# Performance work log

Hardware: AMD Instinct MI355X
Metric: run time of the kernel (lower is better)

Reference implementation:

```python
import jax, jax.numpy as jnp
import numpy as np

NOS = 4          # number of species (experts)
IN = 128         # descriptor size
H1 = 32
H2 = 32
N_ATOMS = 500000


def setup_inputs() -> dict:
    key = jax.random.key(0)
    ks = jax.random.split(key, 8)
    desc = jax.random.normal(ks[0], (N_ATOMS, IN), dtype=jnp.float32)
    species = jax.random.randint(ks[1], (N_ATOMS,), 0, NOS, dtype=jnp.int64)
    s = 0.05  # small init scale
    W0 = jax.random.normal(ks[2], (NOS, IN, H1), dtype=jnp.float32) * s
    b0 = jax.random.normal(ks[3], (NOS, H1), dtype=jnp.float32) * s
    W1 = jax.random.normal(ks[4], (NOS, H1, H2), dtype=jnp.float32) * s
    b1 = jax.random.normal(ks[5], (NOS, H2), dtype=jnp.float32) * s
    W2 = jax.random.normal(ks[6], (NOS, H2, 1), dtype=jnp.float32) * s
    b2 = jax.random.normal(ks[7], (NOS, 1), dtype=jnp.float32) * s
    return {"desc": desc, "species": species, "W0": W0, "b0": b0,
            "W1": W1, "b1": b1, "W2": W2, "b2": b2}


def reference(desc, species, W0, b0, W1, b1, W2, b2):
    # Run every species MLP on all atoms (NOS is small), then select per
    # atom's species and sum -> total energy. Same math as predict_E.
    # h: [s, n, h1]
    h = jnp.tanh(jnp.einsum('ni,sih->snh', desc, W0) + b0[:, None, :])
    h = jnp.tanh(jnp.einsum('snh,sho->sno', h, W1) + b1[:, None, :])
    out = jnp.einsum('snh,sho->sno', h, W2) + b2[:, None, :]   # [s, n, 1]
    per_atom = jnp.take_along_axis(out[..., 0], species[None, :], axis=0)[0]
    return jnp.sum(per_atom)
```

## Files before the change

### kernel.cpp

```cpp
#include <hip/hip_runtime.h>
#include <hip/hip_bf16.h>


#define NATOMS 500000
#define NSPEC  4
#define DIN    128
#define DH1    32
#define DH2    32

#define IDX_CAP 500064
#define T_MAX   (IDX_CAP / 16)

#define OFF_COUNTS 0
#define OFF_CURS   16
#define OFF_BASES  32
#define OFF_IDX    256
#define OFF_FRAG   2000640
#define SPEC_STRIDE 11840

typedef __bf16 bf16x8 __attribute__((ext_vector_type(8)));
typedef float  f32x4  __attribute__((ext_vector_type(4)));

__device__ __forceinline__ float fast_tanh(float x) {
    float e = exp2f(x * 2.8853900817779268f);
    return 1.0f - 2.0f / (e + 1.0f);
}

__global__ void k0_init(char* ws, float* out) {
    int t = threadIdx.x;
    if (t < 4) ((int*)(ws + OFF_COUNTS))[t] = 0;
    if (t == 0) out[0] = 0.0f;
}

__global__ void k1_hist(const int* __restrict__ species, char* ws) {
    __shared__ int h[NSPEC];
    int t = threadIdx.x;
    if (t < NSPEC) h[t] = 0;
    __syncthreads();
    int i = blockIdx.x * blockDim.x + t;
    if (i < NATOMS) {
        int s = species[i];
        atomicAdd(&h[s], 1);
    }
    __syncthreads();
    if (t < NSPEC) atomicAdd((int*)(ws + OFF_COUNTS) + t, h[t]);
}

__global__ void k2_prep(const float* __restrict__ W0, const float* __restrict__ b0,
                        const float* __restrict__ W1, const float* __restrict__ b1,
                        const float* __restrict__ W2, char* ws) {
    int tid = threadIdx.x;
    int* counts = (int*)(ws + OFF_COUNTS);
    int* curs   = (int*)(ws + OFF_CURS);
    int* bases  = (int*)(ws + OFF_BASES);
    int* idx    = (int*)(ws + OFF_IDX);

    if (tid == 0) {
        int b = 0;
        bases[0] = 0;
        for (int s = 0; s < NSPEC; s++) {
            int c = counts[s];
            int a = (c + 15) & ~15;
            curs[s] = b;
            for (int p = b + c; p < b + a; p++) idx[p] = -1;
            b += a;
            bases[s + 1] = b;
        }
        for (int p = b; p < IDX_CAP; p++) idx[p] = -1;
    }

    int s = tid >> 6, l = tid & 63;
    int kg = l >> 4, lo = l & 15;
    char* fb = ws + OFF_FRAG + (size_t)s * SPEC_STRIDE;

    for (int kt = 0; kt < 4; kt++) {
        for (int jt = 0; jt < 2; jt++) {
            bf16x8 v;
            for (int e = 0; e < 8; e++) {
                int k = kt * 32 + kg * 8 + e;
                int j = jt * 16 + lo;
                v[e] = (__bf16)W0[(s * DIN + k) * DH1 + j];
            }
            *(bf16x8*)(fb + (kt * 2 + jt) * 1024 + l * 16) = v;
        }
    }
    for (int jt = 0; jt < 2; jt++) {
        bf16x8 v;
        for (int e = 0; e < 8; e++) {
            int k = kg * 8 + e;
            int j = jt * 16 + lo;
            v[e] = (__bf16)W1[(s * DH1 + k) * DH2 + j];
        }
        *(bf16x8*)(fb + 8192 + jt * 1024 + l * 16) = v;
    }
    for (int jt = 0; jt < 2; jt++) {
        *(float*)(fb + 10240 + (jt * 64 + l) * 4) = b0[s * DH1 + jt * 16 + lo];
        *(float*)(fb + 10752 + (jt * 64 + l) * 4) = b1[s * DH2 + jt * 16 + lo];
        *(float*)(fb + 11264 + (jt * 64 + l) * 4) = W2[s * DH2 + jt * 16 + lo];
    }
}

__global__ void k3_scatter(const int* __restrict__ species, char* ws) {
    __shared__ int h[NSPEC];
    __shared__ int base[NSPEC];
    int t = threadIdx.x;
    if (t < NSPEC) h[t] = 0;
    __syncthreads();
    int i = blockIdx.x * blockDim.x + t;
    int s = 0, r = 0;
    bool ok = (i < NATOMS);
    if (ok) {
        s = species[i];
        r = atomicAdd(&h[s], 1);
    }
    __syncthreads();
    if (t < NSPEC) base[t] = atomicAdd((int*)(ws + OFF_CURS) + t, h[t]);
    __syncthreads();
    if (ok) ((int*)(ws + OFF_IDX))[base[s] + r] = i;
}

__global__ __launch_bounds__(256) void k4_main(const float* __restrict__ desc,
                                               const float* __restrict__ b2,
                                               const char* __restrict__ ws,
                                               float* __restrict__ out) {
    __shared__ alignas(16) __bf16 h1buf[4][16][32];

    const int* bases = (const int*)(ws + OFF_BASES);
    const int* idx   = (const int*)(ws + OFF_IDX);

    int tid = threadIdx.x;
    int l   = tid & 63;
    int w   = tid >> 6;
    int lo  = l & 15;
    int kg  = l >> 4;

    int gw = blockIdx.x * 4 + w;
    int nw = gridDim.x * 4;
    int chunk = (T_MAX + nw - 1) / nw;
    int t0 = gw * chunk;
    int t1 = t0 + chunk; if (t1 > T_MAX) t1 = T_MAX;
    if (t0 >= t1) return;

    int B1 = bases[1], B2 = bases[2], B3 = bases[3];

    int scur = -1;
    bf16x8 w0f[4][2], w1f[2];
    float b0f[2], b1f[2], w2f[2], b2v = 0.0f;
    float esum = 0.0f;

    for (int t = t0; t < t1; t++) {
        int p0 = t * 16;
        int s = (p0 >= B3) ? 3 : (p0 >= B2) ? 2 : (p0 >= B1) ? 1 : 0;
        if (s != scur) {
            const char* fb = ws + OFF_FRAG + (size_t)s * SPEC_STRIDE;
#pragma unroll
            for (int kt = 0; kt < 4; kt++) {
                w0f[kt][0] = *(const bf16x8*)(fb + (kt * 2 + 0) * 1024 + l * 16);
                w0f[kt][1] = *(const bf16x8*)(fb + (kt * 2 + 1) * 1024 + l * 16);
            }
            w1f[0] = *(const bf16x8*)(fb + 8192 + l * 16);
            w1f[1] = *(const bf16x8*)(fb + 8192 + 1024 + l * 16);
            b0f[0] = *(const float*)(fb + 10240 + l * 4);
            b0f[1] = *(const float*)(fb + 10240 + (64 + l) * 4);
            b1f[0] = *(const float*)(fb + 10752 + l * 4);
            b1f[1] = *(const float*)(fb + 10752 + (64 + l) * 4);
            w2f[0] = *(const float*)(fb + 11264 + l * 4);
            w2f[1] = *(const float*)(fb + 11264 + (64 + l) * 4);
            b2v = b2[s];
            scur = s;
        }

        int idxv = idx[p0 + lo];
        int atom = idxv < 0 ? 0 : idxv;
        const float* dp = desc + (size_t)atom * DIN + kg * 8;

        f32x4 acc0 = {0.f, 0.f, 0.f, 0.f}, acc1 = {0.f, 0.f, 0.f, 0.f};
#pragma unroll
        for (int kt = 0; kt < 4; kt++) {
            float4 x = *(const float4*)(dp + kt * 32);
            float4 y = *(const float4*)(dp + kt * 32 + 4);
            bf16x8 a;
            a[0] = (__bf16)x.x; a[1] = (__bf16)x.y; a[2] = (__bf16)x.z; a[3] = (__bf16)x.w;
            a[4] = (__bf16)y.x; a[5] = (__bf16)y.y; a[6] = (__bf16)y.z; a[7] = (__bf16)y.w;
            acc0 = __builtin_amdgcn_mfma_f32_16x16x32_bf16(a, w0f[kt][0], acc0, 0, 0, 0);
            acc1 = __builtin_amdgcn_mfma_f32_16x16x32_bf16(a, w0f[kt][1], acc1, 0, 0, 0);
        }

#pragma unroll
        for (int jt = 0; jt < 2; jt++) {
            float bb = b0f[jt];
#pragma unroll
            for (int r = 0; r < 4; r++) {
                float v = fast_tanh((jt ? acc1[r] : acc0[r]) + bb);
                int roww = kg * 4 + r;
                int col  = jt * 16 + lo;
                int sw   = (col >> 3) ^ (roww & 3) ^ (roww >> 2);
                h1buf[w][roww][sw * 8 + (col & 7)] = (__bf16)v;
            }
        }
        int swr = kg ^ (lo & 3) ^ ((lo >> 2) & 3);
        bf16x8 ha = *(bf16x8*)&h1buf[w][lo][swr * 8];

        f32x4 c10 = {0.f, 0.f, 0.f, 0.f}, c11 = {0.f, 0.f, 0.f, 0.f};
        c10 = __builtin_amdgcn_mfma_f32_16x16x32_bf16(ha, w1f[0], c10, 0, 0, 0);
        c11 = __builtin_amdgcn_mfma_f32_16x16x32_bf16(ha, w1f[1], c11, 0, 0, 0);

        float p[4];
#pragma unroll
        for (int r = 0; r < 4; r++) {
            float h20 = fast_tanh(c10[r] + b1f[0]);
            float h21 = fast_tanh(c11[r] + b1f[1]);
            p[r] = h20 * w2f[0] + h21 * w2f[1];
        }
#pragma unroll
        for (int r = 0; r < 4; r++) {
            p[r] += __shfl_xor(p[r], 1);
            p[r] += __shfl_xor(p[r], 2);
            p[r] += __shfl_xor(p[r], 4);
            p[r] += __shfl_xor(p[r], 8);
        }

        unsigned long long bal = __ballot(idxv >= 0);
        float te = 0.0f;
#pragma unroll
        for (int r = 0; r < 4; r++) {
            int roww = kg * 4 + r;
            if ((bal >> roww) & 1ULL) te += p[r] + b2v;
        }
        te += __shfl_xor(te, 16);
        te += __shfl_xor(te, 32);
        esum += te;
    }
    if (l == 0) atomicAdd(out, esum);
}

extern "C" void kernel_launch(void* const* d_in, const int* in_sizes, int n_in,
                              void* d_out, int out_size, void* d_ws, size_t ws_size,
                              hipStream_t stream) {
    const float* desc    = (const float*)d_in[0];
    const int*   species = (const int*)d_in[1];
    const float* W0      = (const float*)d_in[2];
    const float* b0      = (const float*)d_in[3];
    const float* W1      = (const float*)d_in[4];
    const float* b1      = (const float*)d_in[5];
    const float* W2      = (const float*)d_in[6];
    const float* b2      = (const float*)d_in[7];
    char*  ws  = (char*)d_ws;
    float* out = (float*)d_out;

    int nb = (NATOMS + 1023) / 1024;

    k0_init<<<1, 64, 0, stream>>>(ws, out);
    k1_hist<<<nb, 1024, 0, stream>>>(species, ws);
    k2_prep<<<1, 256, 0, stream>>>(W0, b0, W1, b1, W2, ws);
    k3_scatter<<<nb, 1024, 0, stream>>>(species, ws);
    k4_main<<<1024, 256, 0, stream>>>(desc, b2, ws, out);
}
```

Before: 418.6 us.

## Software-pipeline descriptor loads with interleaved tile assignment in main MLP kernel

```diff
diff --git a/kernel.cpp b/kernel.cpp
--- a/kernel.cpp
+++ b/kernel.cpp
@@ -10,6 +10,10 @@
 
 #define IDX_CAP 500064
 #define T_MAX   (IDX_CAP / 16)
+
+#define K4_BLOCKS 768
+#define K4_WAVES  (K4_BLOCKS * 4)
+#define CHUNK     11
 
 #define OFF_COUNTS 0
 #define OFF_CURS   16
@@ -38,10 +42,7 @@
     if (t < NSPEC) h[t] = 0;
     __syncthreads();
     int i = blockIdx.x * blockDim.x + t;
-    if (i < NATOMS) {
-        int s = species[i];
-        atomicAdd(&h[s], 1);
-    }
+    if (i < NATOMS) atomicAdd(&h[species[i]], 1);
     __syncthreads();
     if (t < NSPEC) atomicAdd((int*)(ws + OFF_COUNTS) + t, h[t]);
 }
@@ -135,11 +136,6 @@
     int kg  = l >> 4;
 
     int gw = blockIdx.x * 4 + w;
-    int nw = gridDim.x * 4;
-    int chunk = (T_MAX + nw - 1) / nw;
-    int t0 = gw * chunk;
-    int t1 = t0 + chunk; if (t1 > T_MAX) t1 = T_MAX;
-    if (t0 >= t1) return;
 
     int B1 = bases[1], B2 = bases[2], B3 = bases[3];
 
@@ -148,90 +144,108 @@
     float b0f[2], b1f[2], w2f[2], b2v = 0.0f;
     float esum = 0.0f;
 
-    for (int t = t0; t < t1; t++) {
-        int p0 = t * 16;
-        int s = (p0 >= B3) ? 3 : (p0 >= B2) ? 2 : (p0 >= B1) ? 1 : 0;
-        if (s != scur) {
-            const char* fb = ws + OFF_FRAG + (size_t)s * SPEC_STRIDE;
-#pragma unroll
-            for (int kt = 0; kt < 4; kt++) {
-                w0f[kt][0] = *(const bf16x8*)(fb + (kt * 2 + 0) * 1024 + l * 16);
-                w0f[kt][1] = *(const bf16x8*)(fb + (kt * 2 + 1) * 1024 + l * 16);
-            }
-            w1f[0] = *(const bf16x8*)(fb + 8192 + l * 16);
-            w1f[1] = *(const bf16x8*)(fb + 8192 + 1024 + l * 16);
-            b0f[0] = *(const float*)(fb + 10240 + l * 4);
-            b0f[1] = *(const float*)(fb + 10240 + (64 + l) * 4);
-            b1f[0] = *(const float*)(fb + 10752 + l * 4);
-            b1f[1] = *(const float*)(fb + 10752 + (64 + l) * 4);
-            w2f[0] = *(const float*)(fb + 11264 + l * 4);
-            w2f[1] = *(const float*)(fb + 11264 + (64 + l) * 4);
-            b2v = b2[s];
-            scur = s;
-        }
-
-        int idxv = idx[p0 + lo];
-        int atom = idxv < 0 ? 0 : idxv;
-        const float* dp = desc + (size_t)atom * DIN + kg * 8;
-
-        f32x4 acc0 = {0.f, 0.f, 0.f, 0.f}, acc1 = {0.f, 0.f, 0.f, 0.f};
-#pragma unroll
-        for (int kt = 0; kt < 4; kt++) {
-            float4 x = *(const float4*)(dp + kt * 32);
-            float4 y = *(const float4*)(dp + kt * 32 + 4);
-            bf16x8 a;
-            a[0] = (__bf16)x.x; a[1] = (__bf16)x.y; a[2] = (__bf16)x.z; a[3] = (__bf16)x.w;
-            a[4] = (__bf16)y.x; a[5] = (__bf16)y.y; a[6] = (__bf16)y.z; a[7] = (__bf16)y.w;
-            acc0 = __builtin_amdgcn_mfma_f32_16x16x32_bf16(a, w0f[kt][0], acc0, 0, 0, 0);
-            acc1 = __builtin_amdgcn_mfma_f32_16x16x32_bf16(a, w0f[kt][1], acc1, 0, 0, 0);
-        }
-
-#pragma unroll
-        for (int jt = 0; jt < 2; jt++) {
-            float bb = b0f[jt];
-#pragma unroll
-            for (int r = 0; r < 4; r++) {
-                float v = fast_tanh((jt ? acc1[r] : acc0[r]) + bb);
-                int roww = kg * 4 + r;
-                int col  = jt * 16 + lo;
-                int sw   = (col >> 3) ^ (roww & 3) ^ (roww >> 2);
-                h1buf[w][roww][sw * 8 + (col & 7)] = (__bf16)v;
-            }
-        }
-        int swr = kg ^ (lo & 3) ^ ((lo >> 2) & 3);
-        bf16x8 ha = *(bf16x8*)&h1buf[w][lo][swr * 8];
-
-        f32x4 c10 = {0.f, 0.f, 0.f, 0.f}, c11 = {0.f, 0.f, 0.f, 0.f};
-        c10 = __builtin_amdgcn_mfma_f32_16x16x32_bf16(ha, w1f[0], c10, 0, 0, 0);
-        c11 = __builtin_amdgcn_mfma_f32_16x16x32_bf16(ha, w1f[1], c11, 0, 0, 0);
-
-        float p[4];
-#pragma unroll
-        for (int r = 0; r < 4; r++) {
-            float h20 = fast_tanh(c10[r] + b1f[0]);
-            float h21 = fast_tanh(c11[r] + b1f[1]);
-            p[r] = h20 * w2f[0] + h21 * w2f[1];
-        }
-#pragma unroll
-        for (int r = 0; r < 4; r++) {
-            p[r] += __shfl_xor(p[r], 1);
-            p[r] += __shfl_xor(p[r], 2);
-            p[r] += __shfl_xor(p[r], 4);
-            p[r] += __shfl_xor(p[r], 8);
-        }
-
-        unsigned long long bal = __ballot(idxv >= 0);
-        float te = 0.0f;
-#pragma unroll
-        for (int r = 0; r < 4; r++) {
-            int roww = kg * 4 + r;
-            if ((bal >> roww) & 1ULL) te += p[r] + b2v;
-        }
-        te += __shfl_xor(te, 16);
-        te += __shfl_xor(te, 32);
-        esum += te;
-    }
+    float4 dA[8], dB[8];
+
+#define IDX_LD(J_) ((gw + (J_) * K4_WAVES) < T_MAX ? idx[(gw + (J_) * K4_WAVES) * 16 + lo] : -1)
+
+#define LOAD8(D_, IIV_) do {                                                  \
+    int atom_ = (IIV_) < 0 ? 0 : (IIV_);                                      \
+    const float* dp_ = desc + (size_t)atom_ * DIN + kg * 8;                   \
+    D_[0] = *(const float4*)(dp_);       D_[1] = *(const float4*)(dp_ + 4);   \
+    D_[2] = *(const float4*)(dp_ + 32);  D_[3] = *(const float4*)(dp_ + 36);  \
+    D_[4] = *(const float4*)(dp_ + 64);  D_[5] = *(const float4*)(dp_ + 68);  \
+    D_[6] = *(const float4*)(dp_ + 96);  D_[7] = *(const float4*)(dp_ + 100); \
+} while (0)
+
+#define COMPUTE(D_, IIV_, T_) do {                                            \
+    int p0_ = (T_) * 16;                                                      \
+    int s_ = (p0_ >= B3) ? 3 : (p0_ >= B2) ? 2 : (p0_ >= B1) ? 1 : 0;         \
+    if (s_ != scur) {                                                         \
+        const char* fb_ = ws + OFF_FRAG + (size_t)s_ * SPEC_STRIDE;           \
+        _Pragma("unroll")                                                     \
+        for (int kt = 0; kt < 4; kt++) {                                      \
+            w0f[kt][0] = *(const bf16x8*)(fb_ + (kt * 2 + 0) * 1024 + l * 16);\
+            w0f[kt][1] = *(const bf16x8*)(fb_ + (kt * 2 + 1) * 1024 + l * 16);\
+        }                                                                     \
+        w1f[0] = *(const bf16x8*)(fb_ + 8192 + l * 16);                       \
+        w1f[1] = *(const bf16x8*)(fb_ + 8192 + 1024 + l * 16);                \
+        b0f[0] = *(const float*)(fb_ + 10240 + l * 4);                        \
+        b0f[1] = *(const float*)(fb_ + 10240 + (64 + l) * 4);                 \
+        b1f[0] = *(const float*)(fb_ + 10752 + l * 4);                        \
+        b1f[1] = *(const float*)(fb_ + 10752 + (64 + l) * 4);                 \
+        w2f[0] = *(const float*)(fb_ + 11264 + l * 4);                        \
+        w2f[1] = *(const float*)(fb_ + 11264 + (64 + l) * 4);                 \
+        b2v = b2[s_];                                                         \
+        scur = s_;                                                            \
+    }                                                                         \
+    f32x4 acc0_ = {0.f,0.f,0.f,0.f}, acc1_ = {0.f,0.f,0.f,0.f};               \
+    _Pragma("unroll")                                                         \
+    for (int kt = 0; kt < 4; kt++) {                                          \
+        float4 x_ = D_[2 * kt], y_ = D_[2 * kt + 1];                          \
+        bf16x8 a_;                                                            \
+        a_[0] = (__bf16)x_.x; a_[1] = (__bf16)x_.y;                           \
+        a_[2] = (__bf16)x_.z; a_[3] = (__bf16)x_.w;                           \
+        a_[4] = (__bf16)y_.x; a_[5] = (__bf16)y_.y;                           \
+        a_[6] = (__bf16)y_.z; a_[7] = (__bf16)y_.w;                           \
+        acc0_ = __builtin_amdgcn_mfma_f32_16x16x32_bf16(a_, w0f[kt][0], acc0_, 0, 0, 0); \
+        acc1_ = __builtin_amdgcn_mfma_f32_16x16x32_bf16(a_, w0f[kt][1], acc1_, 0, 0, 0); \
+    }                                                                         \
+    _Pragma("unroll")                                                         \
+    for (int jt = 0; jt < 2; jt++) {                                          \
+        float bb_ = b0f[jt];                                                  \
+        _Pragma("unroll")                                                     \
+        for (int r = 0; r < 4; r++) {                                         \
+            float v_ = fast_tanh((jt ? acc1_[r] : acc0_[r]) + bb_);           \
+            int roww_ = kg * 4 + r;                                           \
+            int col_  = jt * 16 + lo;                                         \
+            int sw_   = (col_ >> 3) ^ (roww_ & 3) ^ (roww_ >> 2);             \
+            h1buf[w][roww_][sw_ * 8 + (col_ & 7)] = (__bf16)v_;               \
+        }                                                                     \
+    }                                                                         \
+    int swr_ = kg ^ (lo & 3) ^ ((lo >> 2) & 3);                               \
+    bf16x8 ha_ = *(bf16x8*)&h1buf[w][lo][swr_ * 8];                           \
+    f32x4 c10_ = {0.f,0.f,0.f,0.f}, c11_ = {0.f,0.f,0.f,0.f};                 \
+    c10_ = __builtin_amdgcn_mfma_f32_16x16x32_bf16(ha_, w1f[0], c10_, 0, 0, 0); \
+    c11_ = __builtin_amdgcn_mfma_f32_16x16x32_bf16(ha_, w1f[1], c11_, 0, 0, 0); \
+    unsigned long long bal_ = __ballot((IIV_) >= 0);                          \
+    _Pragma("unroll")                                                         \
+    for (int r = 0; r < 4; r++) {                                             \
+        float h20_ = fast_tanh(c10_[r] + b1f[0]);                             \
+        float h21_ = fast_tanh(c11_[r] + b1f[1]);                             \
+        float pp_ = h20_ * w2f[0] + h21_ * w2f[1];                            \
+        if ((bal_ >> (kg * 4 + r)) & 1ULL) esum += pp_;                       \
+    }                                                                         \
+    if (l == 0) esum += (float)__popcll(bal_ & 0xFFFFULL) * b2v;              \
+} while (0)
+
+    int iiA  = IDX_LD(0);
+    int iiB  = IDX_LD(1);
+    int iiN0 = IDX_LD(2);
+    int iiN1 = IDX_LD(3);
+    LOAD8(dA, iiA);
+
+    for (int j = 0; j < CHUNK - 1; j += 2) {
+        LOAD8(dB, iiB);
+        int nn0 = (j + 4 < CHUNK) ? IDX_LD(j + 4) : -1;
+        int nn1 = (j + 5 < CHUNK) ? IDX_LD(j + 5) : -1;
+        COMPUTE(dA, iiA, gw + j * K4_WAVES);
+        LOAD8(dA, iiN0);
+        COMPUTE(dB, iiB, gw + (j + 1) * K4_WAVES);
+        iiA = iiN0; iiB = iiN1; iiN0 = nn0; iiN1 = nn1;
+    }
+    COMPUTE(dA, iiA, gw + (CHUNK - 1) * K4_WAVES);
+
+    esum += __shfl_xor(esum, 1);
+    esum += __shfl_xor(esum, 2);
+    esum += __shfl_xor(esum, 4);
+    esum += __shfl_xor(esum, 8);
+    esum += __shfl_xor(esum, 16);
+    esum += __shfl_xor(esum, 32);
     if (l == 0) atomicAdd(out, esum);
+
+#undef IDX_LD
+#undef LOAD8
+#undef COMPUTE
 }
 
 extern "C" void kernel_launch(void* const* d_in, const int* in_sizes, int n_in,
@@ -254,5 +268,5 @@
     k1_hist<<<nb, 1024, 0, stream>>>(species, ws);
     k2_prep<<<1, 256, 0, stream>>>(W0, b0, W1, b1, W2, ws);
     k3_scatter<<<nb, 1024, 0, stream>>>(species, ws);
-    k4_main<<<1024, 256, 0, stream>>>(desc, b2, ws, out);
-}
+    k4_main<<<K4_BLOCKS, 256, 0, stream>>>(desc, b2, ws, out);
+}
```

Measured after the change: 390.9 us. 6.6% less time.

## Evaluate all species MLPs per contiguous tile instead of sorting atoms by species

Applied to the files above, without the earlier changes.

```diff
diff --git a/kernel.cpp b/kernel.cpp
--- a/kernel.cpp
+++ b/kernel.cpp
@@ -7,90 +7,44 @@
 #define DIN    128
 #define DH1    32
 #define DH2    32
-
-#define IDX_CAP 500064
-#define T_MAX   (IDX_CAP / 16)
-
-#define OFF_COUNTS 0
-#define OFF_CURS   16
-#define OFF_BASES  32
-#define OFF_IDX    256
-#define OFF_FRAG   2000640
-#define SPEC_STRIDE 11840
+#define NTILES (NATOMS / 16)
+
+#define K4_BLOCKS 768
+#define K4_WAVES  (K4_BLOCKS * 4)
+#define CHUNK     ((NTILES + K4_WAVES - 1) / K4_WAVES)
+
+#define SPEC_STRIDE 11776
 
 typedef __bf16 bf16x8 __attribute__((ext_vector_type(8)));
 typedef float  f32x4  __attribute__((ext_vector_type(4)));
 
 __device__ __forceinline__ float fast_tanh(float x) {
-    float e = exp2f(x * 2.8853900817779268f);
-    return 1.0f - 2.0f / (e + 1.0f);
-}
-
-__global__ void k0_init(char* ws, float* out) {
-    int t = threadIdx.x;
-    if (t < 4) ((int*)(ws + OFF_COUNTS))[t] = 0;
-    if (t == 0) out[0] = 0.0f;
-}
-
-__global__ void k1_hist(const int* __restrict__ species, char* ws) {
-    __shared__ int h[NSPEC];
-    int t = threadIdx.x;
-    if (t < NSPEC) h[t] = 0;
-    __syncthreads();
-    int i = blockIdx.x * blockDim.x + t;
-    if (i < NATOMS) {
-        int s = species[i];
-        atomicAdd(&h[s], 1);
-    }
-    __syncthreads();
-    if (t < NSPEC) atomicAdd((int*)(ws + OFF_COUNTS) + t, h[t]);
-}
-
-__global__ void k2_prep(const float* __restrict__ W0, const float* __restrict__ b0,
-                        const float* __restrict__ W1, const float* __restrict__ b1,
-                        const float* __restrict__ W2, char* ws) {
+    float e = __builtin_amdgcn_exp2f(x * 2.8853900817779268f);
+    return 1.0f - 2.0f * __builtin_amdgcn_rcpf(e + 1.0f);
+}
+
+__global__ void kprep(const float* __restrict__ W0, const float* __restrict__ b0,
+                      const float* __restrict__ W1, const float* __restrict__ b1,
+                      const float* __restrict__ W2, char* ws, float* out) {
     int tid = threadIdx.x;
-    int* counts = (int*)(ws + OFF_COUNTS);
-    int* curs   = (int*)(ws + OFF_CURS);
-    int* bases  = (int*)(ws + OFF_BASES);
-    int* idx    = (int*)(ws + OFF_IDX);
-
-    if (tid == 0) {
-        int b = 0;
-        bases[0] = 0;
-        for (int s = 0; s < NSPEC; s++) {
-            int c = counts[s];
-            int a = (c + 15) & ~15;
-            curs[s] = b;
-            for (int p = b + c; p < b + a; p++) idx[p] = -1;
-            b += a;
-            bases[s + 1] = b;
-        }
-        for (int p = b; p < IDX_CAP; p++) idx[p] = -1;
-    }
+    if (tid == 0) out[0] = 0.0f;
 
     int s = tid >> 6, l = tid & 63;
     int kg = l >> 4, lo = l & 15;
-    char* fb = ws + OFF_FRAG + (size_t)s * SPEC_STRIDE;
+    char* fb = ws + (size_t)s * SPEC_STRIDE;
 
     for (int kt = 0; kt < 4; kt++) {
         for (int jt = 0; jt < 2; jt++) {
             bf16x8 v;
-            for (int e = 0; e < 8; e++) {
-                int k = kt * 32 + kg * 8 + e;
-                int j = jt * 16 + lo;
-                v[e] = (__bf16)W0[(s * DIN + k) * DH1 + j];
-            }
+            for (int e = 0; e < 8; e++)
+                v[e] = (__bf16)W0[(s * DIN + kt * 32 + kg * 8 + e) * DH1 + jt * 16 + lo];
             *(bf16x8*)(fb + (kt * 2 + jt) * 1024 + l * 16) = v;
         }
     }
     for (int jt = 0; jt < 2; jt++) {
         bf16x8 v;
-        for (int e = 0; e < 8; e++) {
-            int k = kg * 8 + e;
-            int j = jt * 16 + lo;
-            v[e] = (__bf16)W1[(s * DH1 + k) * DH2 + j];
-        }
+        for (int e = 0; e < 8; e++)
+            v[e] = (__bf16)W1[(s * DH1 + kg * 8 + e) * DH2 + jt * 16 + lo];
         *(bf16x8*)(fb + 8192 + jt * 1024 + l * 16) = v;
     }
     for (int jt = 0; jt < 2; jt++) {
@@ -100,137 +54,130 @@
     }
 }
 
-__global__ void k3_scatter(const int* __restrict__ species, char* ws) {
-    __shared__ int h[NSPEC];
-    __shared__ int base[NSPEC];
-    int t = threadIdx.x;
-    if (t < NSPEC) h[t] = 0;
+__global__ __launch_bounds__(256) void k4_all(const float* __restrict__ desc,
+                                              const int* __restrict__ species,
+                                              const float* __restrict__ b2g,
+                                              const char* __restrict__ ws,
+                                              float* __restrict__ out) {
+    __shared__ __align__(16) char w0lds[4 * 8192];
+    __shared__ __align__(16) __bf16 h1buf[4][16][32];
+
+    int tid = threadIdx.x, l = tid & 63, w = tid >> 6;
+    int lo = l & 15, kg = l >> 4;
+
+    for (int s = 0; s < 4; s++) {
+#pragma unroll
+        for (int i = 0; i < 2; i++) {
+            int off = (i * 256 + tid) * 16;
+            *(float4*)(w0lds + s * 8192 + off) =
+                *(const float4*)(ws + (size_t)s * SPEC_STRIDE + off);
+        }
+    }
     __syncthreads();
-    int i = blockIdx.x * blockDim.x + t;
-    int s = 0, r = 0;
-    bool ok = (i < NATOMS);
-    if (ok) {
-        s = species[i];
-        r = atomicAdd(&h[s], 1);
-    }
-    __syncthreads();
-    if (t < NSPEC) base[t] = atomicAdd((int*)(ws + OFF_CURS) + t, h[t]);
-    __syncthreads();
-    if (ok) ((int*)(ws + OFF_IDX))[base[s] + r] = i;
-}
-
-__global__ __launch_bounds__(256) void k4_main(const float* __restrict__ desc,
-                                               const float* __restrict__ b2,
-                                               const char* __restrict__ ws,
-                                               float* __restrict__ out) {
-    __shared__ alignas(16) __bf16 h1buf[4][16][32];
-
-    const int* bases = (const int*)(ws + OFF_BASES);
-    const int* idx   = (const int*)(ws + OFF_IDX);
-
-    int tid = threadIdx.x;
-    int l   = tid & 63;
-    int w   = tid >> 6;
-    int lo  = l & 15;
-    int kg  = l >> 4;
+
+    bf16x8 w1f[4][2];
+    float  b0f[4][2], b1f[4][2], w2f[4][2], b2v[4];
+#pragma unroll
+    for (int s = 0; s < 4; s++) {
+        const char* fb = ws + (size_t)s * SPEC_STRIDE;
+        w1f[s][0] = *(const bf16x8*)(fb + 8192 + l * 16);
+        w1f[s][1] = *(const bf16x8*)(fb + 8192 + 1024 + l * 16);
+        b0f[s][0] = *(const float*)(fb + 10240 + l * 4);
+        b0f[s][1] = *(const float*)(fb + 10240 + (64 + l) * 4);
+        b1f[s][0] = *(const float*)(fb + 10752 + l * 4);
+        b1f[s][1] = *(const float*)(fb + 10752 + (64 + l) * 4);
+        w2f[s][0] = *(const float*)(fb + 11264 + l * 4);
+        w2f[s][1] = *(const float*)(fb + 11264 + (64 + l) * 4);
+        b2v[s]    = b2g[s];
+    }
 
     int gw = blockIdx.x * 4 + w;
-    int nw = gridDim.x * 4;
-    int chunk = (T_MAX + nw - 1) / nw;
-    int t0 = gw * chunk;
-    int t1 = t0 + chunk; if (t1 > T_MAX) t1 = T_MAX;
-    if (t0 >= t1) return;
-
-    int B1 = bases[1], B2 = bases[2], B3 = bases[3];
-
-    int scur = -1;
-    bf16x8 w0f[4][2], w1f[2];
-    float b0f[2], b1f[2], w2f[2], b2v = 0.0f;
+    int t0 = gw * CHUNK;
+    int t1 = t0 + CHUNK; if (t1 > NTILES) t1 = NTILES;
     float esum = 0.0f;
 
-    for (int t = t0; t < t1; t++) {
-        int p0 = t * 16;
-        int s = (p0 >= B3) ? 3 : (p0 >= B2) ? 2 : (p0 >= B1) ? 1 : 0;
-        if (s != scur) {
-            const char* fb = ws + OFF_FRAG + (size_t)s * SPEC_STRIDE;
+#define LOAD8(T_) do {                                                        \
+    const float* dp_ = desc + ((size_t)(T_) * 16 + lo) * DIN + kg * 8;        \
+    dA[0] = *(const float4*)(dp_);       dA[1] = *(const float4*)(dp_ + 4);   \
+    dA[2] = *(const float4*)(dp_ + 32);  dA[3] = *(const float4*)(dp_ + 36);  \
+    dA[4] = *(const float4*)(dp_ + 64);  dA[5] = *(const float4*)(dp_ + 68);  \
+    dA[6] = *(const float4*)(dp_ + 96);  dA[7] = *(const float4*)(dp_ + 100); \
+} while (0)
+
+    if (t0 < t1) {
+        float4 dA[8];
+        LOAD8(t0);
+        for (int t = t0; t < t1; ++t) {
+            bf16x8 a[4];
 #pragma unroll
             for (int kt = 0; kt < 4; kt++) {
-                w0f[kt][0] = *(const bf16x8*)(fb + (kt * 2 + 0) * 1024 + l * 16);
-                w0f[kt][1] = *(const bf16x8*)(fb + (kt * 2 + 1) * 1024 + l * 16);
+                float4 x = dA[2 * kt], y = dA[2 * kt + 1];
+                bf16x8 aa;
+                aa[0] = (__bf16)x.x; aa[1] = (__bf16)x.y;
+                aa[2] = (__bf16)x.z; aa[3] = (__bf16)x.w;
+                aa[4] = (__bf16)y.x; aa[5] = (__bf16)y.y;
+                aa[6] = (__bf16)y.z; aa[7] = (__bf16)y.w;
+                a[kt] = aa;
             }
-            w1f[0] = *(const bf16x8*)(fb + 8192 + l * 16);
-            w1f[1] = *(const bf16x8*)(fb + 8192 + 1024 + l * 16);
-            b0f[0] = *(const float*)(fb + 10240 + l * 4);
-            b0f[1] = *(const float*)(fb + 10240 + (64 + l) * 4);
-            b1f[0] = *(const float*)(fb + 10752 + l * 4);
-            b1f[1] = *(const float*)(fb + 10752 + (64 + l) * 4);
-            w2f[0] = *(const float*)(fb + 11264 + l * 4);
-            w2f[1] = *(const float*)(fb + 11264 + (64 + l) * 4);
-            b2v = b2[s];
-            scur = s;
-        }
-
-        int idxv = idx[p0 + lo];
-        int atom = idxv < 0 ? 0 : idxv;
-        const float* dp = desc + (size_t)atom * DIN + kg * 8;
-
-        f32x4 acc0 = {0.f, 0.f, 0.f, 0.f}, acc1 = {0.f, 0.f, 0.f, 0.f};
-#pragma unroll
-        for (int kt = 0; kt < 4; kt++) {
-            float4 x = *(const float4*)(dp + kt * 32);
-            float4 y = *(const float4*)(dp + kt * 32 + 4);
-            bf16x8 a;
-            a[0] = (__bf16)x.x; a[1] = (__bf16)x.y; a[2] = (__bf16)x.z; a[3] = (__bf16)x.w;
-            a[4] = (__bf16)y.x; a[5] = (__bf16)y.y; a[6] = (__bf16)y.z; a[7] = (__bf16)y.w;
-            acc0 = __builtin_amdgcn_mfma_f32_16x16x32_bf16(a, w0f[kt][0], acc0, 0, 0, 0);
-            acc1 = __builtin_amdgcn_mfma_f32_16x16x32_bf16(a, w0f[kt][1], acc1, 0, 0, 0);
-        }
-
-#pragma unroll
-        for (int jt = 0; jt < 2; jt++) {
-            float bb = b0f[jt];
-#pragma unroll
-            for (int r = 0; r < 4; r++) {
-                float v = fast_tanh((jt ? acc1[r] : acc0[r]) + bb);
-                int roww = kg * 4 + r;
-                int col  = jt * 16 + lo;
-                int sw   = (col >> 3) ^ (roww & 3) ^ (roww >> 2);
-                h1buf[w][roww][sw * 8 + (col & 7)] = (__bf16)v;
+            if (t + 1 < t1) LOAD8(t + 1);
+
+            int p0 = t * 16;
+            int sv = species[p0 + lo];
+            int spr0 = __shfl(sv, kg * 4 + 0);
+            int spr1 = __shfl(sv, kg * 4 + 1);
+            int spr2 = __shfl(sv, kg * 4 + 2);
+            int spr3 = __shfl(sv, kg * 4 + 3);
+
+#pragma unroll
+            for (int sp = 0; sp < 4; sp++) {
+                f32x4 acc0 = {0.f, 0.f, 0.f, 0.f}, acc1 = {0.f, 0.f, 0.f, 0.f};
+#pragma unroll
+                for (int kt = 0; kt < 4; kt++) {
+                    bf16x8 bv0 = *(const bf16x8*)(w0lds + sp * 8192 + (kt * 2 + 0) * 1024 + l * 16);
+                    bf16x8 bv1 = *(const bf16x8*)(w0lds + sp * 8192 + (kt * 2 + 1) * 1024 + l * 16);
+                    acc0 = __builtin_amdgcn_mfma_f32_16x16x32_bf16(a[kt], bv0, acc0, 0, 0, 0);
+                    acc1 = __builtin_amdgcn_mfma_f32_16x16x32_bf16(a[kt], bv1, acc1, 0, 0, 0);
+                }
+#pragma unroll
+                for (int jt = 0; jt < 2; jt++) {
+                    float bb = b0f[sp][jt];
+#pragma unroll
+                    for (int r = 0; r < 4; r++) {
+                        float v = fast_tanh((jt ? acc1[r] : acc0[r]) + bb);
+                        int roww = kg * 4 + r;
+                        int col  = jt * 16 + lo;
+                        int sw   = (col >> 3) ^ (roww & 3) ^ (roww >> 2);
+                        h1buf[w][roww][sw * 8 + (col & 7)] = (__bf16)v;
+                    }
+                }
+                int swr = kg ^ (lo & 3) ^ ((lo >> 2) & 3);
+                bf16x8 ha = *(bf16x8*)&h1buf[w][lo][swr * 8];
+
+                f32x4 c10 = {0.f, 0.f, 0.f, 0.f}, c11 = {0.f, 0.f, 0.f, 0.f};
+                c10 = __builtin_amdgcn_mfma_f32_16x16x32_bf16(ha, w1f[sp][0], c10, 0, 0, 0);
+                c11 = __builtin_amdgcn_mfma_f32_16x16x32_bf16(ha, w1f[sp][1], c11, 0, 0, 0);
+
+#pragma unroll
+                for (int r = 0; r < 4; r++) {
+                    int spr = (r == 0) ? spr0 : (r == 1) ? spr1 : (r == 2) ? spr2 : spr3;
+                    if (spr == sp) {
+                        float h20 = fast_tanh(c10[r] + b1f[sp][0]);
+                        float h21 = fast_tanh(c11[r] + b1f[sp][1]);
+                        esum += h20 * w2f[sp][0] + h21 * w2f[sp][1];
+                        if (lo == 0) esum += b2v[sp];
+                    }
+                }
             }
         }
-        int swr = kg ^ (lo & 3) ^ ((lo >> 2) & 3);
-        bf16x8 ha = *(bf16x8*)&h1buf[w][lo][swr * 8];
-
-        f32x4 c10 = {0.f, 0.f, 0.f, 0.f}, c11 = {0.f, 0.f, 0.f, 0.f};
-        c10 = __builtin_amdgcn_mfma_f32_16x16x32_bf16(ha, w1f[0], c10, 0, 0, 0);
-        c11 = __builtin_amdgcn_mfma_f32_16x16x32_bf16(ha, w1f[1], c11, 0, 0, 0);
-
-        float p[4];
-#pragma unroll
-        for (int r = 0; r < 4; r++) {
-            float h20 = fast_tanh(c10[r] + b1f[0]);
-            float h21 = fast_tanh(c11[r] + b1f[1]);
-            p[r] = h20 * w2f[0] + h21 * w2f[1];
-        }
-#pragma unroll
-        for (int r = 0; r < 4; r++) {
-            p[r] += __shfl_xor(p[r], 1);
-            p[r] += __shfl_xor(p[r], 2);
-            p[r] += __shfl_xor(p[r], 4);
-            p[r] += __shfl_xor(p[r], 8);
-        }
-
-        unsigned long long bal = __ballot(idxv >= 0);
-        float te = 0.0f;
-#pragma unroll
-        for (int r = 0; r < 4; r++) {
-            int roww = kg * 4 + r;
-            if ((bal >> roww) & 1ULL) te += p[r] + b2v;
-        }
-        te += __shfl_xor(te, 16);
-        te += __shfl_xor(te, 32);
-        esum += te;
-    }
+    }
+#undef LOAD8
+
+    esum += __shfl_xor(esum, 1);
+    esum += __shfl_xor(esum, 2);
+    esum += __shfl_xor(esum, 4);
+    esum += __shfl_xor(esum, 8);
+    esum += __shfl_xor(esum, 16);
+    esum += __shfl_xor(esum, 32);
     if (l == 0) atomicAdd(out, esum);
 }
 
@@ -248,11 +195,6 @@
     char*  ws  = (char*)d_ws;
     float* out = (float*)d_out;
 
-    int nb = (NATOMS + 1023) / 1024;
-
-    k0_init<<<1, 64, 0, stream>>>(ws, out);
-    k1_hist<<<nb, 1024, 0, stream>>>(species, ws);
-    k2_prep<<<1, 256, 0, stream>>>(W0, b0, W1, b1, W2, ws);
-    k3_scatter<<<nb, 1024, 0, stream>>>(species, ws);
-    k4_main<<<1024, 256, 0, stream>>>(desc, b2, ws, out);
-}
+    kprep<<<1, 256, 0, stream>>>(W0, b0, W1, b1, W2, ws, out);
+    k4_all<<<K4_BLOCKS, 256, 0, stream>>>(desc, species, b2, ws, out);
+}
```

Measured after the change: 397.0 us. -5.2%, faster.
